# Kernel optimization log

Hardware: AMD Instinct MI355X
Metric: run time of the kernel (lower is better)

Reference implementation:

```python
import jax, jax.numpy as jnp
import numpy as np
import math

H = 4            # cross_attn_heads
SPARSE_RATIO = 0.6
B, N, C = 128, 196, 768


def setup_inputs() -> dict:
    key = jax.random.key(0)
    ks = jax.random.split(key, 10)
    xav = (6.0 / (C + C)) ** 0.5  # xavier_uniform bound for square Linear
    inp = {
        "RGB_cash": jax.random.normal(ks[0], (B, N, C), jnp.float32),
        "NI_cash": jax.random.normal(ks[1], (B, N, C), jnp.float32),
        "TI_cash": jax.random.normal(ks[2], (B, N, C), jnp.float32),
        "RGB_global": jax.random.normal(ks[3], (B, C), jnp.float32),
        "NI_global": jax.random.normal(ks[4], (B, C), jnp.float32),
        "TI_global": jax.random.normal(ks[5], (B, C), jnp.float32),
        # 9 CrossModalAttention modules, stacked: q_proj / k_proj weights (out,in) and biases
        "q_w": jax.random.uniform(ks[6], (9, C, C), jnp.float32, -xav, xav),
        "q_b": jnp.zeros((9, C), jnp.float32),
        "k_w": jax.random.uniform(ks[7], (9, C, C), jnp.float32, -xav, xav),
        "k_b": jnp.zeros((9, C), jnp.float32),
        # 3 TokenSparse modal_weights, init torch.ones(3); small noise for non-degenerate softmax
        "modal_w": jnp.ones((3, 3), jnp.float32) + 0.01 * jax.random.normal(ks[8], (3, 3), jnp.float32),
    }
    return inp


def _cos_sim(patches, g):
    # patches (B,N,C), g (B,C) -> (B,N); F.normalize eps=1e-12
    pn = patches / jnp.maximum(jnp.linalg.norm(patches, axis=-1, keepdims=True), 1e-12)
    gn = g / jnp.maximum(jnp.linalg.norm(g, axis=-1, keepdims=True), 1e-12)
    return jnp.einsum("bnc,bc->bn", pn, gn)


def _cross_attn(patches, g, cos, qw, qb, kw, kb):
    # CrossModalAttention.forward: Q from global (1 token), K from patches, softmax over N
    b, n, c = patches.shape
    d = c // H
    q = (g @ qw.T + qb).reshape(b, H, d)              # (B,H,D)
    k = (patches @ kw.T + kb).reshape(b, n, H, d)     # (B,N,H,D)
    attn = jnp.einsum("bhd,bnhd->bhn", q, k) * (d ** -0.5)
    attn = jax.nn.softmax(attn, axis=-1)              # (B,H,N)
    return (attn * cos[:, None, :]).mean(axis=1)      # (B,N)


def _minmax(s):
    smin = s.min(axis=-1, keepdims=True)
    smax = s.max(axis=-1, keepdims=True)
    return (s - smin) / (smax - smin + 1e-8)


def _token_sparse(tokens, s_im, s_m2, s_m3, mw):
    b, n, c = tokens.shape
    w = jax.nn.softmax(mw)
    score = w[0] * _minmax(s_im) + w[1] * _minmax(s_m2) + w[2] * _minmax(s_m3)
    num_keep = max(1, math.ceil(n * SPARSE_RATIO))
    _, idx = jax.lax.top_k(score, num_keep)           # == descending sort, first num_keep
    mask = jnp.zeros((b, n), score.dtype).at[jnp.arange(b)[:, None], idx].set(1.0)
    return tokens * mask[..., None], mask


def reference(RGB_cash, NI_cash, TI_cash, RGB_global, NI_global, TI_global,
              q_w, q_b, k_w, k_b, modal_w):
    toks = [RGB_cash, NI_cash, TI_cash]
    glbs = [RGB_global, NI_global, TI_global]
    # module order: rgb_self, rgb_x_nir, rgb_x_tir, nir_self, nir_x_rgb, nir_x_tir,
    #               tir_self, tir_x_rgb, tir_x_nir
    order = [(0, 0), (0, 1), (0, 2), (1, 1), (1, 0), (1, 2), (2, 2), (2, 0), (2, 1)]
    scores = []
    for i, (pi, gi) in enumerate(order):
        cos = _cos_sim(toks[pi], glbs[gi])
        scores.append(_cross_attn(toks[pi], glbs[gi], cos, q_w[i], q_b[i], k_w[i], k_b[i]))
    out_rgb, m_rgb = _token_sparse(RGB_cash, scores[0], scores[1], scores[2], modal_w[0])
    out_nir, m_nir = _token_sparse(NI_cash, scores[3], scores[4], scores[5], modal_w[1])
    out_tir, m_tir = _token_sparse(TI_cash, scores[6], scores[7], scores[8], modal_w[2])
    return (out_rgb, out_nir, out_tir, m_rgb, m_nir, m_tir)
```

## Files before the change

kernel.cpp:

```cpp
#include <hip/hip_runtime.h>
#include <math.h>

#define BB   128
#define NN   196
#define CC   768
#define HH   4
#define DD   192
#define TOK_PER   19267584
#define NUM_KEEP  118
#define SCALE_D   0.07216878364870322f

#define OFF_QPART 0
#define SZ_QPART  (2*9*128*768)
#define OFF_VV    (OFF_QPART + SZ_QPART)
#define SZ_VV     (9*128*4*768)
#define OFF_SC    (OFF_VV + SZ_VV)
#define SZ_SC     (3*128*196*16)

__device__ __forceinline__ float4 f4fma(float s, float4 b, float4 a) {
  a.x = fmaf(s, b.x, a.x); a.y = fmaf(s, b.y, a.y);
  a.z = fmaf(s, b.z, a.z); a.w = fmaf(s, b.w, a.w);
  return a;
}
__device__ __forceinline__ float f4dot(float4 p, float4 q) {
  return p.x*q.x + p.y*q.y + p.z*q.z + p.w*q.w;
}

__global__ __launch_bounds__(256) void k_qproj(const float* __restrict__ g0,
                                               const float* __restrict__ g1,
                                               const float* __restrict__ g2,
                                               const float* __restrict__ qw,
                                               float* __restrict__ qpart) {
  __shared__ __align__(16) float AsT[32 * 68];
  __shared__ __align__(16) float WsT[32 * 68];
  const int gtab[9] = {0, 1, 2, 1, 0, 2, 2, 0, 1};
  int i = blockIdx.y, z = blockIdx.z;
  int mt = blockIdx.x & 1, nt = blockIdx.x >> 1;
  int tid = threadIdx.x, tx = tid & 15, ty = tid >> 4;
  int gi = gtab[i];
  const float4* A4 = (const float4*)((gi == 0) ? g0 : ((gi == 1) ? g1 : g2));
  const float4* W4 = (const float4*)(qw + (size_t)i * CC * CC);
  float4 acc0 = {0,0,0,0}, acc1 = {0,0,0,0}, acc2 = {0,0,0,0}, acc3 = {0,0,0,0};
  int arow = mt * 64, wrow = nt * 64;
  int kb4 = z * 96;
  for (int kk = 0; kk < 12; kk++) {
    #pragma unroll
    for (int f = tid; f < 512; f += 256) {
      int r = f >> 3, k4 = f & 7;
      float4 va = A4[(size_t)(arow + r) * 192 + kb4 + kk * 8 + k4];
      float4 vw = W4[(size_t)(wrow + r) * 192 + kb4 + kk * 8 + k4];
      int kq = 4 * k4;
      AsT[(kq+0)*68 + r] = va.x; AsT[(kq+1)*68 + r] = va.y;
      AsT[(kq+2)*68 + r] = va.z; AsT[(kq+3)*68 + r] = va.w;
      WsT[(kq+0)*68 + r] = vw.x; WsT[(kq+1)*68 + r] = vw.y;
      WsT[(kq+2)*68 + r] = vw.z; WsT[(kq+3)*68 + r] = vw.w;
    }
    __syncthreads();
    #pragma unroll
    for (int k = 0; k < 32; k++) {
      float4 a = *(const float4*)&AsT[k * 68 + 4 * ty];
      float4 w = *(const float4*)&WsT[k * 68 + 4 * tx];
      acc0 = f4fma(a.x, w, acc0); acc1 = f4fma(a.y, w, acc1);
      acc2 = f4fma(a.z, w, acc2); acc3 = f4fma(a.w, w, acc3);
    }
    __syncthreads();
  }
  float* dst = qpart + (size_t)(z * 9 + i) * 128 * CC;
  int col = wrow + 4 * tx;
  int row = arow + 4 * ty;
  *(float4*)&dst[(size_t)(row + 0) * CC + col] = acc0;
  *(float4*)&dst[(size_t)(row + 1) * CC + col] = acc1;
  *(float4*)&dst[(size_t)(row + 2) * CC + col] = acc2;
  *(float4*)&dst[(size_t)(row + 3) * CC + col] = acc3;
}

__global__ __launch_bounds__(256) void k_vvproj(const float* __restrict__ qpart,
                                                const float* __restrict__ qb,
                                                const float* __restrict__ kw,
                                                float* __restrict__ vvout) {
  __shared__ __align__(16) float AsT[32 * 68];
  __shared__ __align__(16) float Bs[32 * 68];
  int ih = blockIdx.y; int i = ih >> 2, h = ih & 3;
  int mt = blockIdx.x & 1, nt = blockIdx.x >> 1;
  int tid = threadIdx.x, tx = tid & 15, ty = tid >> 4;
  const float4* qp0 = (const float4*)qpart + (size_t)i * 128 * 192;
  const float4* qp1 = (const float4*)qpart + (size_t)(9 + i) * 128 * 192;
  const float4* qb4 = (const float4*)qb + (size_t)i * 192;
  const float4* B4  = (const float4*)(kw + (size_t)i * CC * CC);
  float4 acc0 = {0,0,0,0}, acc1 = {0,0,0,0}, acc2 = {0,0,0,0}, acc3 = {0,0,0,0};
  int arow = mt * 64;
  int bcol4 = nt * 16;
  for (int kk = 0; kk < 6; kk++) {
    #pragma unroll
    for (int f = tid; f < 512; f += 256) {
      int r = f >> 3, k4 = f & 7;
      int colf4 = h * 48 + kk * 8 + k4;
      float4 va = qp0[(size_t)(arow + r) * 192 + colf4];
      float4 vb = qp1[(size_t)(arow + r) * 192 + colf4];
      float4 vq = qb4[colf4];
      va.x += vb.x + vq.x; va.y += vb.y + vq.y;
      va.z += vb.z + vq.z; va.w += vb.w + vq.w;
      int kq = 4 * k4;
      AsT[(kq+0)*68 + r] = va.x; AsT[(kq+1)*68 + r] = va.y;
      AsT[(kq+2)*68 + r] = va.z; AsT[(kq+3)*68 + r] = va.w;
      int rk = f >> 4, c4 = f & 15;
      float4 vB = B4[(size_t)(h * DD + kk * 32 + rk) * 192 + bcol4 + c4];
      *(float4*)&Bs[rk * 68 + 4 * c4] = vB;
    }
    __syncthreads();
    #pragma unroll
    for (int k = 0; k < 32; k++) {
      float4 a = *(const float4*)&AsT[k * 68 + 4 * ty];
      float4 bb = *(const float4*)&Bs[k * 68 + 4 * tx];
      acc0 = f4fma(a.x, bb, acc0); acc1 = f4fma(a.y, bb, acc1);
      acc2 = f4fma(a.z, bb, acc2); acc3 = f4fma(a.w, bb, acc3);
    }
    __syncthreads();
  }
  int col = nt * 64 + 4 * tx;
  int b0 = arow + 4 * ty;
  *(float4*)&vvout[((size_t)(i * 128 + b0 + 0) * 4 + h) * CC + col] = acc0;
  *(float4*)&vvout[((size_t)(i * 128 + b0 + 1) * 4 + h) * CC + col] = acc1;
  *(float4*)&vvout[((size_t)(i * 128 + b0 + 2) * 4 + h) * CC + col] = acc2;
  *(float4*)&vvout[((size_t)(i * 128 + b0 + 3) * 4 + h) * CC + col] = acc3;
}

__global__ __launch_bounds__(256, 2) void k_dots(const float* __restrict__ rgb,
                                                 const float* __restrict__ ni,
                                                 const float* __restrict__ ti,
                                                 const float* __restrict__ vv,
                                                 const float* __restrict__ g0,
                                                 const float* __restrict__ g1,
                                                 const float* __restrict__ g2,
                                                 const float* __restrict__ qpart,
                                                 const float* __restrict__ qb,
                                                 const float* __restrict__ kb,
                                                 float* __restrict__ sc,
                                                 float* __restrict__ out) {
  __shared__ float red[4][64 * 17];
  __shared__ __align__(16) float GN[3 * CC];
  __shared__ float BIASs[12];
  int bid = blockIdx.x;
  int t = bid >> 8;
  int rem = bid & 255;
  int b = rem >> 1, half = rem & 1;
  int tid = threadIdx.x;
  int w = tid >> 6, lane = tid & 63;
  const float* toks = (t == 0) ? rgb : ((t == 1) ? ni : ti);
  int gi0, gi1, gi2;
  if (t == 0)      { gi0 = 0; gi1 = 1; gi2 = 2; }
  else if (t == 1) { gi0 = 1; gi1 = 0; gi2 = 2; }
  else             { gi0 = 2; gi1 = 0; gi2 = 1; }

  float4 V[36];
  #pragma unroll
  for (int k = 0; k < 3; k++) {
    #pragma unroll
    for (int h = 0; h < 4; h++) {
      const float4* src = (const float4*)(vv + (((size_t)(3*t + k) * 128 + b) * 4 + h) * CC);
      int v = k * 4 + h;
      V[3*v + 0] = src[lane];
      V[3*v + 1] = src[lane + 64];
      V[3*v + 2] = src[lane + 128];
    }
  }

  if (w < 3) {
    int gidx = (w == 0) ? gi0 : ((w == 1) ? gi1 : gi2);
    const float* gsrc = (gidx == 0) ? g0 : ((gidx == 1) ? g1 : g2);
    const float4* s4 = (const float4*)(gsrc + (size_t)b * CC);
    float4 u0 = s4[lane], u1 = s4[lane + 64], u2 = s4[lane + 128];
    float ss = f4dot(u0, u0) + f4dot(u1, u1) + f4dot(u2, u2);
    #pragma unroll
    for (int off = 32; off; off >>= 1) ss += __shfl_xor(ss, off);
    float inv = 1.0f / fmaxf(sqrtf(ss), 1e-12f);
    u0.x *= inv; u0.y *= inv; u0.z *= inv; u0.w *= inv;
    u1.x *= inv; u1.y *= inv; u1.z *= inv; u1.w *= inv;
    u2.x *= inv; u2.y *= inv; u2.z *= inv; u2.w *= inv;
    float4* d4 = (float4*)&GN[w * CC];
    d4[lane] = u0; d4[lane + 64] = u1; d4[lane + 128] = u2;

    int i = 3 * t + w;
    const float* qbb = qb + (size_t)i * CC;
    const float* kbb = kb + (size_t)i * CC;
    const float* q0p = qpart + ((size_t)i * 128 + b) * CC;
    const float* q1p = qpart + ((size_t)(9 + i) * 128 + b) * CC;
    #pragma unroll
    for (int h = 0; h < 4; h++) {
      int j0 = h * DD + lane;
      float s = (q0p[j0]       + q1p[j0]       + qbb[j0])       * kbb[j0]
              + (q0p[j0 + 64]  + q1p[j0 + 64]  + qbb[j0 + 64])  * kbb[j0 + 64]
              + (q0p[j0 + 128] + q1p[j0 + 128] + qbb[j0 + 128]) * kbb[j0 + 128];
      #pragma unroll
      for (int off = 32; off; off >>= 1) s += __shfl_xor(s, off);
      if (lane == 0) BIASs[w * 4 + h] = s;
    }
  }
  __syncthreads();

  int a_id = lane & 15;
  float bias_r = (a_id < 12) ? BIASs[a_id] : 0.f;

  float* myred = red[w];
  const float4* G4 = (const float4*)GN;
  int s_grp = lane >> 4;
  int n0 = half * 98;
  float* obase = out + ((size_t)t * 128 + b) * NN * CC;

  const float4* pr0 = (const float4*)(toks + ((size_t)b * NN + n0 + w) * CC);
  float4 pc0 = pr0[lane], pc1 = pr0[lane + 64], pc2 = pr0[lane + 128];

  for (int it = 0; it < 25; it++) {
    int row_local = it * 4 + w;
    if (row_local >= 98) break;
    int n = n0 + row_local;

    int rl_next = row_local + 4;
    float4 pn0 = pc0, pn1 = pc1, pn2 = pc2;
    if (rl_next < 98) {
      const float4* pr = (const float4*)(toks + ((size_t)b * NN + n0 + rl_next) * CC);
      pn0 = pr[lane]; pn1 = pr[lane + 64]; pn2 = pr[lane + 128];
    }

    float a[16];
    #pragma unroll
    for (int v = 0; v < 12; v++)
      a[v] = f4dot(pc0, V[3*v]) + f4dot(pc1, V[3*v + 1]) + f4dot(pc2, V[3*v + 2]);
    #pragma unroll
    for (int j = 0; j < 3; j++)
      a[12 + j] = f4dot(pc0, G4[j*192 + lane])
                + f4dot(pc1, G4[j*192 + lane + 64])
                + f4dot(pc2, G4[j*192 + lane + 128]);
    a[15] = f4dot(pc0, pc0) + f4dot(pc1, pc1) + f4dot(pc2, pc2);

    {
      float4* dstr = (float4*)(obase + (size_t)n * CC);
      dstr[lane] = pc0; dstr[lane + 64] = pc1; dstr[lane + 128] = pc2;
    }

    #pragma unroll
    for (int v = 0; v < 16; v++) myred[lane * 17 + v] = a[v];
    __builtin_amdgcn_s_waitcnt(0xc07f);
    __builtin_amdgcn_sched_barrier(0);
    float part = 0.f;
    #pragma unroll
    for (int i2 = 0; i2 < 16; i2++)
      part += myred[(s_grp * 16 + i2) * 17 + a_id];
    part += __shfl_xor(part, 16, 64);
    part += __shfl_xor(part, 32, 64);

    float s15  = __shfl(part, 15, 64);
    float invp = 1.0f / fmaxf(sqrtf(s15), 1e-12f);
    float res;
    if (a_id < 12)      res = (part + bias_r) * SCALE_D;
    else if (a_id < 15) res = part * invp;
    else                res = invp;

    if (lane < 16) {
      float* scrow = sc + (((size_t)t * 128 + b) * 196 + n) * 16;
      scrow[lane] = res;
    }
    pc0 = pn0; pc1 = pn1; pc2 = pn2;
  }
}

__global__ __launch_bounds__(256) void k_mask(const float* __restrict__ sc,
                                              const float* __restrict__ modal_w,
                                              float* __restrict__ out,
                                              float* __restrict__ outmask) {
  __shared__ float S[196 * 17];
  __shared__ float CSUM[12];
  __shared__ float SV[3][196];
  __shared__ float MN[3], MX[3];
  __shared__ float sfinal[196];
  __shared__ float keepf[196];
  int b = blockIdx.x, m = blockIdx.y;
  int tid = threadIdx.x;
  int w = tid >> 6, lane = tid & 63;
  bool act = tid < NN;

  const float4* base = (const float4*)(sc + ((size_t)m * 128 + b) * 196 * 16);
  if (act) {
    float4 r0 = base[tid*4+0], r1 = base[tid*4+1], r2 = base[tid*4+2], r3 = base[tid*4+3];
    float* d = &S[tid * 17];
    d[0] = r0.x; d[1] = r0.y; d[2]  = r0.z; d[3]  = r0.w;
    d[4] = r1.x; d[5] = r1.y; d[6]  = r1.z; d[7]  = r1.w;
    d[8] = r2.x; d[9] = r2.y; d[10] = r2.z; d[11] = r2.w;
    d[12] = r3.x; d[13] = r3.y; d[14] = r3.z;
  }
  __syncthreads();

  #pragma unroll
  for (int c = w; c < 12; c += 4) {
    int n3 = lane + 192;
    float v0 = S[(lane      ) * 17 + c];
    float v1 = S[(lane +  64) * 17 + c];
    float v2 = S[(lane + 128) * 17 + c];
    float v3 = (n3 < NN) ? S[n3 * 17 + c] : -3.4e38f;
    float mx = fmaxf(fmaxf(v0, v1), fmaxf(v2, v3));
    #pragma unroll
    for (int off = 32; off; off >>= 1) mx = fmaxf(mx, __shfl_xor(mx, off));
    float e0 = expf(v0 - mx), e1 = expf(v1 - mx), e2 = expf(v2 - mx);
    float e3 = (n3 < NN) ? expf(v3 - mx) : 0.f;
    float es = e0 + e1 + e2 + e3;
    #pragma unroll
    for (int off = 32; off; off >>= 1) es += __shfl_xor(es, off);
    S[(lane      ) * 17 + c] = e0;
    S[(lane +  64) * 17 + c] = e1;
    S[(lane + 128) * 17 + c] = e2;
    if (n3 < NN) S[n3 * 17 + c] = e3;
    if (lane == 0) CSUM[c] = es;
  }
  __syncthreads();

  float scv0 = 0.f, scv1 = 0.f, scv2 = 0.f;
  if (act) {
    const float* r = &S[tid * 17];
    float as0 = r[0]/CSUM[0] + r[1]/CSUM[1] + r[2]/CSUM[2]  + r[3]/CSUM[3];
    float as1 = r[4]/CSUM[4] + r[5]/CSUM[5] + r[6]/CSUM[6]  + r[7]/CSUM[7];
    float as2 = r[8]/CSUM[8] + r[9]/CSUM[9] + r[10]/CSUM[10] + r[11]/CSUM[11];
    scv0 = r[12] * as0 * 0.25f;
    scv1 = r[13] * as1 * 0.25f;
    scv2 = r[14] * as2 * 0.25f;
    SV[0][tid] = scv0; SV[1][tid] = scv1; SV[2][tid] = scv2;
  }
  __syncthreads();

  if (w < 3) {
    float u0 = SV[w][lane], u1 = SV[w][lane + 64], u2 = SV[w][lane + 128];
    float mn = fminf(fminf(u0, u1), u2);
    float mx = fmaxf(fmaxf(u0, u1), u2);
    if (lane + 192 < NN) {
      float u3 = SV[w][lane + 192];
      mn = fminf(mn, u3); mx = fmaxf(mx, u3);
    }
    #pragma unroll
    for (int off = 32; off; off >>= 1) {
      mn = fminf(mn, __shfl_xor(mn, off));
      mx = fmaxf(mx, __shfl_xor(mx, off));
    }
    if (lane == 0) { MN[w] = mn; MX[w] = mx; }
  }
  __syncthreads();

  float w0 = modal_w[m * 3 + 0], w1 = modal_w[m * 3 + 1], w2 = modal_w[m * 3 + 2];
  float wm = fmaxf(w0, fmaxf(w1, w2));
  float ew0 = expf(w0 - wm), ew1 = expf(w1 - wm), ew2 = expf(w2 - wm);
  float esum = ew0 + ew1 + ew2;
  float fv = 0.f;
  if (act) {
    fv = (ew0 / esum) * (scv0 - MN[0]) / (MX[0] - MN[0] + 1e-8f)
       + (ew1 / esum) * (scv1 - MN[1]) / (MX[1] - MN[1] + 1e-8f)
       + (ew2 / esum) * (scv2 - MN[2]) / (MX[2] - MN[2] + 1e-8f);
    sfinal[tid] = fv;
  }
  __syncthreads();

  if (act) {
    int cnt = 0;
    for (int j = 0; j < NN; j++) {
      float fj = sfinal[j];
      cnt += (fj > fv) || (fj == fv && j < tid);
    }
    float kf = (cnt < NUM_KEEP) ? 1.0f : 0.0f;
    keepf[tid] = kf;
    outmask[((size_t)m * 128 + b) * NN + tid] = kf;
  }
  __syncthreads();

  float* obase = out + ((size_t)m * 128 + b) * NN * CC;
  float4 z = {0.f, 0.f, 0.f, 0.f};
  for (int r = w; r < NN; r += 4) {
    if (keepf[r] == 0.0f) {
      float4* dstr = (float4*)(obase + (size_t)r * CC);
      dstr[lane] = z; dstr[lane + 64] = z; dstr[lane + 128] = z;
    }
  }
}

extern "C" void kernel_launch(void* const* d_in, const int* in_sizes, int n_in,
                              void* d_out, int out_size, void* d_ws, size_t ws_size,
                              hipStream_t stream) {
  const float* rgb = (const float*)d_in[0];
  const float* ni  = (const float*)d_in[1];
  const float* ti  = (const float*)d_in[2];
  const float* g0  = (const float*)d_in[3];
  const float* g1  = (const float*)d_in[4];
  const float* g2  = (const float*)d_in[5];
  const float* qw  = (const float*)d_in[6];
  const float* qb  = (const float*)d_in[7];
  const float* kw  = (const float*)d_in[8];
  const float* kb  = (const float*)d_in[9];
  const float* mw  = (const float*)d_in[10];

  float* ws    = (float*)d_ws;
  float* qpart = ws + OFF_QPART;
  float* vv    = ws + OFF_VV;
  float* sc    = ws + OFF_SC;
  float* outf  = (float*)d_out;
  float* maskb = outf + (size_t)3 * TOK_PER;

  k_qproj<<<dim3(24, 9, 2), 256, 0, stream>>>(g0, g1, g2, qw, qpart);
  k_vvproj<<<dim3(24, 36), 256, 0, stream>>>(qpart, qb, kw, vv);
  k_dots<<<768, 256, 0, stream>>>(rgb, ni, ti, vv, g0, g1, g2,
                                  qpart, qb, kb, sc, outf);
  k_mask<<<dim3(128, 3), 256, 0, stream>>>(sc, mw, outf, maskb);
}
```

Baseline: 526.8 us.

## Split dot-product work across waves by head group using shared row tiles

Restructures k_dots so that each wave holds only 12 float4 vectors in registers: waves 0-2 each compute the four head dots for one attention module, and wave 3 computes the three cosine dots and the norm. Groups of four token rows are loaded cooperatively into a double-buffered LDS tile and shared by all waves, in place of each wave streaming its own row. This cuts register pressure from the 36-vector V array, which could raise occupancy, and removes the GN shared array. In exchange it adds a __syncthreads per 4-row group and LDS traffic for the row tile, and wave 3 does less arithmetic than the other waves, leaving the work unbalanced.

```diff
diff --git a/kernel.cpp b/kernel.cpp
--- a/kernel.cpp
+++ b/kernel.cpp
@@ -137,9 +137,10 @@
                                                  const float* __restrict__ kb,
                                                  float* __restrict__ sc,
                                                  float* __restrict__ out) {
+  __shared__ __align__(16) float4 ROW[2][4 * 192];
   __shared__ float red[4][64 * 17];
-  __shared__ __align__(16) float GN[3 * CC];
   __shared__ float BIASs[12];
+
   int bid = blockIdx.x;
   int t = bid >> 8;
   int rem = bid & 255;
@@ -152,35 +153,16 @@
   else if (t == 1) { gi0 = 1; gi1 = 0; gi2 = 2; }
   else             { gi0 = 2; gi1 = 0; gi2 = 1; }
 
-  float4 V[36];
-  #pragma unroll
-  for (int k = 0; k < 3; k++) {
+  float4 V[12];
+  if (w < 3) {
+    int i = 3 * t + w;
     #pragma unroll
     for (int h = 0; h < 4; h++) {
-      const float4* src = (const float4*)(vv + (((size_t)(3*t + k) * 128 + b) * 4 + h) * CC);
-      int v = k * 4 + h;
-      V[3*v + 0] = src[lane];
-      V[3*v + 1] = src[lane + 64];
-      V[3*v + 2] = src[lane + 128];
-    }
-  }
-
-  if (w < 3) {
-    int gidx = (w == 0) ? gi0 : ((w == 1) ? gi1 : gi2);
-    const float* gsrc = (gidx == 0) ? g0 : ((gidx == 1) ? g1 : g2);
-    const float4* s4 = (const float4*)(gsrc + (size_t)b * CC);
-    float4 u0 = s4[lane], u1 = s4[lane + 64], u2 = s4[lane + 128];
-    float ss = f4dot(u0, u0) + f4dot(u1, u1) + f4dot(u2, u2);
-    #pragma unroll
-    for (int off = 32; off; off >>= 1) ss += __shfl_xor(ss, off);
-    float inv = 1.0f / fmaxf(sqrtf(ss), 1e-12f);
-    u0.x *= inv; u0.y *= inv; u0.z *= inv; u0.w *= inv;
-    u1.x *= inv; u1.y *= inv; u1.z *= inv; u1.w *= inv;
-    u2.x *= inv; u2.y *= inv; u2.z *= inv; u2.w *= inv;
-    float4* d4 = (float4*)&GN[w * CC];
-    d4[lane] = u0; d4[lane + 64] = u1; d4[lane + 128] = u2;
-
-    int i = 3 * t + w;
+      const float4* src = (const float4*)(vv + (((size_t)i * 128 + b) * 4 + h) * CC);
+      V[3*h + 0] = src[lane];
+      V[3*h + 1] = src[lane + 64];
+      V[3*h + 2] = src[lane + 128];
+    }
     const float* qbb = qb + (size_t)i * CC;
     const float* kbb = kb + (size_t)i * CC;
     const float* q0p = qpart + ((size_t)i * 128 + b) * CC;
@@ -195,47 +177,80 @@
       for (int off = 32; off; off >>= 1) s += __shfl_xor(s, off);
       if (lane == 0) BIASs[w * 4 + h] = s;
     }
-  }
+  } else {
+    #pragma unroll
+    for (int j = 0; j < 3; j++) {
+      int gidx = (j == 0) ? gi0 : ((j == 1) ? gi1 : gi2);
+      const float* gsrc = (gidx == 0) ? g0 : ((gidx == 1) ? g1 : g2);
+      const float4* s4 = (const float4*)(gsrc + (size_t)b * CC);
+      float4 u0 = s4[lane], u1 = s4[lane + 64], u2 = s4[lane + 128];
+      float ss = f4dot(u0, u0) + f4dot(u1, u1) + f4dot(u2, u2);
+      #pragma unroll
+      for (int off = 32; off; off >>= 1) ss += __shfl_xor(ss, off);
+      float inv = 1.0f / fmaxf(sqrtf(ss), 1e-12f);
+      u0.x *= inv; u0.y *= inv; u0.z *= inv; u0.w *= inv;
+      u1.x *= inv; u1.y *= inv; u1.z *= inv; u1.w *= inv;
+      u2.x *= inv; u2.y *= inv; u2.z *= inv; u2.w *= inv;
+      V[3*j + 0] = u0; V[3*j + 1] = u1; V[3*j + 2] = u2;
+    }
+    V[9] = V[10] = V[11] = make_float4(0.f, 0.f, 0.f, 0.f);
+  }
+
+  int f0 = tid, f1 = tid + 256, f2 = tid + 512;
+  int r0 = f0 / 192, r1 = f1 / 192, r2 = f2 / 192;
+  int c0 = f0 - r0 * 192, c1 = f1 - r1 * 192, c2 = f2 - r2 * 192;
+  int n0 = half * 98;
+  const float4* tok4 = (const float4*)toks + ((size_t)b * NN + n0) * 192;
+  float4* out4 = (float4*)out + (((size_t)t * 128 + b) * NN + n0) * 192;
+  float* scb = sc + (((size_t)t * 128 + b) * 196 + n0) * 16;
+
+  float4 L0 = tok4[r0 * 192 + c0];
+  float4 L1 = tok4[r1 * 192 + c1];
+  float4 L2 = tok4[r2 * 192 + c2];
+  ROW[0][f0] = L0; ROW[0][f1] = L1; ROW[0][f2] = L2;
+  out4[r0 * 192 + c0] = L0;
+  out4[r1 * 192 + c1] = L1;
+  out4[r2 * 192 + c2] = L2;
   __syncthreads();
 
   int a_id = lane & 15;
-  float bias_r = (a_id < 12) ? BIASs[a_id] : 0.f;
-
+  float bias_r = (w < 3) ? BIASs[w * 4 + (lane & 3)] : 0.f;
   float* myred = red[w];
-  const float4* G4 = (const float4*)GN;
   int s_grp = lane >> 4;
-  int n0 = half * 98;
-  float* obase = out + ((size_t)t * 128 + b) * NN * CC;
-
-  const float4* pr0 = (const float4*)(toks + ((size_t)b * NN + n0 + w) * CC);
-  float4 pc0 = pr0[lane], pc1 = pr0[lane + 64], pc2 = pr0[lane + 128];
-
-  for (int it = 0; it < 25; it++) {
-    int row_local = it * 4 + w;
-    if (row_local >= 98) break;
-    int n = n0 + row_local;
-
-    int rl_next = row_local + 4;
-    float4 pn0 = pc0, pn1 = pc1, pn2 = pc2;
-    if (rl_next < 98) {
-      const float4* pr = (const float4*)(toks + ((size_t)b * NN + n0 + rl_next) * CC);
-      pn0 = pr[lane]; pn1 = pr[lane + 64]; pn2 = pr[lane + 128];
+  int buf = 0;
+
+  for (int g = 0; g < 25; g++) {
+    int gb = 4 * (g + 1);
+    bool ld = (g < 24);
+    if (ld) {
+      if (gb + r0 < 98) L0 = tok4[(gb + r0) * 192 + c0];
+      if (gb + r1 < 98) L1 = tok4[(gb + r1) * 192 + c1];
+      if (gb + r2 < 98) L2 = tok4[(gb + r2) * 192 + c2];
     }
 
     float a[16];
-    #pragma unroll
-    for (int v = 0; v < 12; v++)
-      a[v] = f4dot(pc0, V[3*v]) + f4dot(pc1, V[3*v + 1]) + f4dot(pc2, V[3*v + 2]);
-    #pragma unroll
-    for (int j = 0; j < 3; j++)
-      a[12 + j] = f4dot(pc0, G4[j*192 + lane])
-                + f4dot(pc1, G4[j*192 + lane + 64])
-                + f4dot(pc2, G4[j*192 + lane + 128]);
-    a[15] = f4dot(pc0, pc0) + f4dot(pc1, pc1) + f4dot(pc2, pc2);
-
-    {
-      float4* dstr = (float4*)(obase + (size_t)n * CC);
-      dstr[lane] = pc0; dstr[lane + 64] = pc1; dstr[lane + 128] = pc2;
+    const float4* rb = ROW[buf];
+    if (w < 3) {
+      #pragma unroll
+      for (int r = 0; r < 4; r++) {
+        float4 p0 = rb[r * 192 + lane];
+        float4 p1 = rb[r * 192 + lane + 64];
+        float4 p2 = rb[r * 192 + lane + 128];
+        #pragma unroll
+        for (int h = 0; h < 4; h++)
+          a[4*r + h] = f4dot(p0, V[3*h]) + f4dot(p1, V[3*h + 1]) + f4dot(p2, V[3*h + 2]);
+      }
+    } else {
+      #pragma unroll
+      for (int r = 0; r < 4; r++) {
+        float4 p0 = rb[r * 192 + lane];
+        float4 p1 = rb[r * 192 + lane + 64];
+        float4 p2 = rb[r * 192 + lane + 128];
+        #pragma unroll
+        for (int j = 0; j < 3; j++)
+          a[4*r + j] = f4dot(p0, V[3*j]) + f4dot(p1, V[3*j + 1]) + f4dot(p2, V[3*j + 2]);
+        a[4*r + 3] = f4dot(p0, p0) + f4dot(p1, p1) + f4dot(p2, p2);
+      }
     }
 
     #pragma unroll
@@ -249,18 +264,26 @@
     part += __shfl_xor(part, 16, 64);
     part += __shfl_xor(part, 32, 64);
 
-    float s15  = __shfl(part, 15, 64);
-    float invp = 1.0f / fmaxf(sqrtf(s15), 1e-12f);
     float res;
-    if (a_id < 12)      res = (part + bias_r) * SCALE_D;
-    else if (a_id < 15) res = part * invp;
-    else                res = invp;
-
-    if (lane < 16) {
-      float* scrow = sc + (((size_t)t * 128 + b) * 196 + n) * 16;
-      scrow[lane] = res;
-    }
-    pc0 = pn0; pc1 = pn1; pc2 = pn2;
+    if (w < 3) {
+      res = (part + bias_r) * SCALE_D;
+    } else {
+      float s15 = __shfl(part, (lane & 60) | 3, 64);
+      float invp = 1.0f / fmaxf(sqrtf(s15), 1e-12f);
+      res = ((a_id & 3) < 3) ? part * invp : invp;
+    }
+    int rloc = 4 * g + (a_id >> 2);
+    if (lane < 16 && rloc < 98)
+      scb[rloc * 16 + w * 4 + (a_id & 3)] = res;
+
+    if (ld) {
+      float4* wb = ROW[buf ^ 1];
+      if (gb + r0 < 98) { wb[f0] = L0; out4[(gb + r0) * 192 + c0] = L0; }
+      if (gb + r1 < 98) { wb[f1] = L1; out4[(gb + r1) * 192 + c1] = L1; }
+      if (gb + r2 < 98) { wb[f2] = L2; out4[(gb + r2) * 192 + c2] = L2; }
+    }
+    __syncthreads();
+    buf ^= 1;
   }
 }
 
```

Measured after the change: 611.3 us. +16.0%, slower.
